# Kernel tuning notes

Measured on AMD Instinct MI355X. Metric: run time of the kernel, lower is better.

## Reference

```python
import jax, jax.numpy as jnp
import numpy as np

L, S, N, E, H = 2048, 2048, 4, 1024, 16
D = E // H


def setup_inputs() -> dict:
    k0 = jax.random.key(0)
    ks = jax.random.split(k0, 11)
    std = 1.0 / np.sqrt(E)
    return {
        "query": jax.random.normal(ks[0], (L, N, E), jnp.float32),
        "key": jax.random.normal(ks[1], (S, N, E), jnp.float32),
        "value": jax.random.normal(ks[2], (S, N, E), jnp.float32),
        "Wq": jax.random.normal(ks[3], (E, E), jnp.float32) * std,
        "bq": jnp.zeros((E,), jnp.float32),
        "Wk": jax.random.normal(ks[4], (E, E), jnp.float32) * std,
        "bk": jnp.zeros((E,), jnp.float32),
        "Wv": jax.random.normal(ks[5], (E, E), jnp.float32) * std,
        "bv": jnp.zeros((E,), jnp.float32),
        "Wo": jax.random.normal(ks[6], (E, E), jnp.float32) * std,
        "bo": jnp.zeros((E,), jnp.float32),
    }


def reference(query, key, value, Wq, bq, Wk, bk, Wv, bv, Wo, bo):
    # projections (torch Linear: x @ W.T + b)
    q = query @ Wq.T + bq  # [L,N,E]
    k = key @ Wk.T + bk    # [S,N,E]
    v = value @ Wv.T + bv  # [S,N,E]
    # split heads -> [N,H,len,D]
    q = q.reshape(L, N, H, D).transpose(1, 2, 0, 3)
    k = k.reshape(S, N, H, D).transpose(1, 2, 0, 3)
    v = v.reshape(S, N, H, D).transpose(1, 2, 0, 3)
    scores = jnp.einsum("nhld,nhsd->nhls", q, k) / np.sqrt(D).astype(np.float32)
    attn_weights = jax.nn.softmax(scores, axis=-1)  # [N,H,L,S]
    out = jnp.einsum("nhls,nhsd->nhld", attn_weights, v)  # [N,H,L,D]
    out = out.transpose(2, 0, 1, 3).reshape(L, N, E)
    attn_output = out @ Wo.T + bo  # [L,N,E]
    # need_weights=True, average_attn_weights=True -> mean over heads
    return attn_output, attn_weights.mean(axis=1)
```

## Files before the change

### kernel.cpp

```cpp
#include <hip/hip_runtime.h>
#include <hip/hip_bf16.h>

typedef __attribute__((ext_vector_type(8))) short short8;
typedef __attribute__((ext_vector_type(4))) float f32x4;

#define AS1 __attribute__((address_space(1)))
#define AS3 __attribute__((address_space(3)))

__device__ __forceinline__ void gload16(const void* g, void* l) {
  __builtin_amdgcn_global_load_lds((const AS1 unsigned int*)g,
                                   (AS3 unsigned int*)l, 16, 0, 0);
}

__device__ __forceinline__ unsigned short f2bf(float x) {
  unsigned u = __float_as_uint(x);
  u = (u + 0x7FFFu + ((u >> 16) & 1u)) >> 16;
  return (unsigned short)u;
}

__device__ __forceinline__ short8 lds8(const unsigned short* p) {
  return *(const short8*)p;
}

__device__ __forceinline__ short8 lds8s(const unsigned short* base, int row, int byteInRow) {
  const int a = (row << 7) + (byteInRow ^ ((row & 7) << 4));
  return *(const short8*)((const char*)base + a);
}

#define LL 2048
#define NB 4
#define EE 1024
#define HH 16
#define DD 64
#define MROWS 8192
#define SC2 0.18033688f
#define MFIX 16.0f

__global__ __launch_bounds__(256) void conv_bf16(const float* __restrict__ src,
                                                 unsigned short* __restrict__ dst) {
  int i = blockIdx.x * 256 + threadIdx.x;
  float4 v = ((const float4*)src)[i];
  ushort4 o;
  o.x = f2bf(v.x); o.y = f2bf(v.y); o.z = f2bf(v.z); o.w = f2bf(v.w);
  ((ushort4*)dst)[i] = o;
}

__global__ __launch_bounds__(256) void conv_w4(const float* __restrict__ s0,
                                               const float* __restrict__ s1,
                                               const float* __restrict__ s2,
                                               const float* __restrict__ s3,
                                               unsigned short* __restrict__ d0,
                                               unsigned short* __restrict__ d1,
                                               unsigned short* __restrict__ d2,
                                               unsigned short* __restrict__ d3) {
  const float* src;
  unsigned short* dst;
  switch (blockIdx.y) {
    case 0: src = s0; dst = d0; break;
    case 1: src = s1; dst = d1; break;
    case 2: src = s2; dst = d2; break;
    default: src = s3; dst = d3; break;
  }
  int i = blockIdx.x * 256 + threadIdx.x;
  float4 v = ((const float4*)src)[i];
  ushort4 o;
  o.x = f2bf(v.x); o.y = f2bf(v.y); o.z = f2bf(v.z); o.w = f2bf(v.w);
  ((ushort4*)dst)[i] = o;
}

template <int MODE>
__global__ __launch_bounds__(256) void gemm_bt(const unsigned short* __restrict__ A,
                                               const unsigned short* __restrict__ B,
                                               const float* __restrict__ bias,
                                               unsigned short* __restrict__ outb,
                                               float* __restrict__ outf) {
  constexpr int K = 1024;
  __shared__ __align__(16) unsigned short As[2][64 * 64];
  __shared__ __align__(16) unsigned short Bs[2][64 * 64];
  const int tid = threadIdx.x;
  const int lane = tid & 63, w = tid >> 6;
  const int wr = w >> 1, wc = w & 1;
  const int lrow = lane & 15, lg = lane >> 4;
  const int m0 = blockIdx.y * 128, n0 = blockIdx.x * 128;

  f32x4 acc[4][4] = {};

  const int sr = tid >> 3, sseg = tid & 7;
  const int slog = sseg ^ (sr & 7);
  const int mA = sr + 64 * (slog >> 2);
  const int kof = (slog & 3) * 8;
  const unsigned short* ga  = A + (size_t)(m0 + mA) * K + kof;
  const unsigned short* ga2 = A + (size_t)(m0 + mA + 32) * K + kof;
  const unsigned short* gb  = B + (size_t)(n0 + mA) * K + kof;
  const unsigned short* gb2 = B + (size_t)(n0 + mA + 32) * K + kof;

  gload16(ga,  (char*)As[0] + tid * 16);
  gload16(ga2, (char*)As[0] + tid * 16 + 4096);
  gload16(gb,  (char*)Bs[0] + tid * 16);
  gload16(gb2, (char*)Bs[0] + tid * 16 + 4096);
  __syncthreads();

  int cur = 0;
  for (int k0 = 0; k0 < K; k0 += 32) {
    if (k0 + 32 < K) {
      const int nxt = cur ^ 1;
      gload16(ga  + k0 + 32, (char*)As[nxt] + tid * 16);
      gload16(ga2 + k0 + 32, (char*)As[nxt] + tid * 16 + 4096);
      gload16(gb  + k0 + 32, (char*)Bs[nxt] + tid * 16);
      gload16(gb2 + k0 + 32, (char*)Bs[nxt] + tid * 16 + 4096);
    }

    short8 af[4], bfr[4];
#pragma unroll
    for (int mt = 0; mt < 4; ++mt)
      af[mt] = lds8s(As[cur], mt * 16 + lrow, (wr * 4 + lg) * 16);
#pragma unroll
    for (int nt = 0; nt < 4; ++nt)
      bfr[nt] = lds8s(Bs[cur], nt * 16 + lrow, (wc * 4 + lg) * 16);
#pragma unroll
    for (int mt = 0; mt < 4; ++mt)
#pragma unroll
      for (int nt = 0; nt < 4; ++nt)
        acc[mt][nt] = __builtin_amdgcn_mfma_f32_16x16x32_bf16(af[mt], bfr[nt],
                                                              acc[mt][nt], 0, 0, 0);
    __syncthreads();
    cur ^= 1;
  }

#pragma unroll
  for (int mt = 0; mt < 4; ++mt) {
#pragma unroll
    for (int nt = 0; nt < 4; ++nt) {
      const int col = n0 + wc * 64 + nt * 16 + lrow;
      const float bv = bias[col];
#pragma unroll
      for (int r = 0; r < 4; ++r) {
        const int row = m0 + wr * 64 + mt * 16 + lg * 4 + r;
        const float v = acc[mt][nt][r] + bv;
        if (MODE == 0) {
          const int l = row >> 2, n = row & 3, h = col >> 6, d = col & 63;
          outb[(((size_t)(n * HH + h)) * LL + l) * DD + d] = f2bf(v);
        } else if (MODE == 1) {
          const int s = row >> 2, n = row & 3, h = col >> 6, d = col & 63;
          outb[(((size_t)(n * HH + h)) * DD + d) * LL + s] = f2bf(v);
        } else {
          outf[(size_t)row * EE + col] = v;
        }
      }
    }
  }
}

__global__ __launch_bounds__(256) void flash_attn(const unsigned short* __restrict__ qh,
                                                  const unsigned short* __restrict__ kh,
                                                  const unsigned short* __restrict__ vth,
                                                  unsigned short* __restrict__ oh,
                                                  float* __restrict__ cT) {
  __shared__ __align__(16) unsigned short Ks[64 * 64];
  __shared__ __align__(16) unsigned short Vts[64 * 64];
  __shared__ __align__(16) unsigned short QPs[128 * 64];
  const int tid = threadIdx.x, lane = tid & 63, w = tid >> 6;
  const int lrow = lane & 15, lg = lane >> 4;
  const int flat = blockIdx.x + (blockIdx.y << 4);
  const int nh = ((flat >> 7) << 3) | (flat & 7);
  const int l0 = ((flat >> 3) & 15) * 128;

  const unsigned short* qbase = qh + ((size_t)nh * LL + l0) * DD;
  const unsigned short* kbase = kh + (size_t)nh * LL * DD;
  const unsigned short* vbase = vth + (size_t)nh * DD * LL;

  const int sr = tid >> 3;
  const int cs = ((tid & 7) ^ (sr & 7)) * 8;

#pragma unroll
  for (int c = 0; c < 4; ++c)
    gload16(qbase + (size_t)(c * 32 + sr) * DD + cs, (char*)QPs + c * 4096 + tid * 16);
  gload16(kbase + (size_t)sr * DD + cs,        (char*)Ks + tid * 16);
  gload16(kbase + (size_t)(sr + 32) * DD + cs, (char*)Ks + tid * 16 + 4096);
  gload16(vbase + (size_t)sr * LL + cs,        (char*)Vts + tid * 16);
  gload16(vbase + (size_t)(sr + 32) * LL + cs, (char*)Vts + tid * 16 + 4096);
  __syncthreads();

  short8 qa[2][2];
#pragma unroll
  for (int qs = 0; qs < 2; ++qs) {
    qa[qs][0] = lds8s(QPs, w * 32 + qs * 16 + lrow, lg * 16);
    qa[qs][1] = lds8s(QPs, w * 32 + qs * 16 + lrow, 64 + lg * 16);
  }

  const short onev = (short)0x3F80;
  const short8 ones = {onev, onev, onev, onev, onev, onev, onev, onev};
  const f32x4 fz = {};

  f32x4 acco[2][4] = {};
  f32x4 accz[2] = {};

  const unsigned short* kpre = kbase + (size_t)(64 + sr) * DD + cs;
  const unsigned short* vpre = vbase + (size_t)sr * LL + 64 + cs;

  const int prow0 = w * 32 + lrow;

#pragma unroll 1
  for (int t = 0; t < 32; ++t) {
    const bool pf = (t < 31);

    f32x4 sc0[4];
    __builtin_amdgcn_s_setprio(1);
#pragma unroll
    for (int ct = 0; ct < 4; ++ct) {
      short8 b0 = lds8s(Ks, ct * 16 + lrow, lg * 16);
      short8 b1 = lds8s(Ks, ct * 16 + lrow, 64 + lg * 16);
      sc0[ct] = __builtin_amdgcn_mfma_f32_16x16x32_bf16(
          b1, qa[0][1],
          __builtin_amdgcn_mfma_f32_16x16x32_bf16(b0, qa[0][0], fz, 0, 0, 0),
          0, 0, 0);
    }
    __builtin_amdgcn_s_setprio(0);

#pragma unroll
    for (int ct = 0; ct < 4; ++ct) {
      float e0 = __builtin_exp2f(__builtin_fmaf(sc0[ct][0], SC2, -MFIX));
      float e1 = __builtin_exp2f(__builtin_fmaf(sc0[ct][1], SC2, -MFIX));
      float e2 = __builtin_exp2f(__builtin_fmaf(sc0[ct][2], SC2, -MFIX));
      float e3 = __builtin_exp2f(__builtin_fmaf(sc0[ct][3], SC2, -MFIX));
      unsigned int p0, p1;
      asm("v_cvt_pk_bf16_f32 %0, %1, %2" : "=v"(p0) : "v"(e0), "v"(e1));
      asm("v_cvt_pk_bf16_f32 %0, %1, %2" : "=v"(p1) : "v"(e2), "v"(e3));
      const int a = (prow0 << 7) + ((((ct * 2 + (lg >> 1)) ^ (prow0 & 7)) << 4) | ((lg & 1) << 3));
      uint2 u; u.x = p0; u.y = p1;
      *(uint2*)((char*)QPs + a) = u;
    }

    f32x4 sc1[4];
    __builtin_amdgcn_s_setprio(1);
#pragma unroll
    for (int ct = 0; ct < 4; ++ct) {
      short8 b0 = lds8s(Ks, ct * 16 + lrow, lg * 16);
      short8 b1 = lds8s(Ks, ct * 16 + lrow, 64 + lg * 16);
      sc1[ct] = __builtin_amdgcn_mfma_f32_16x16x32_bf16(
          b1, qa[1][1],
          __builtin_amdgcn_mfma_f32_16x16x32_bf16(b0, qa[1][0], fz, 0, 0, 0),
          0, 0, 0);
    }
    __builtin_amdgcn_s_setprio(0);

    __syncthreads();
    if (pf) {
      gload16(kpre,                   (char*)Ks + tid * 16);
      gload16(kpre + (size_t)32 * DD, (char*)Ks + tid * 16 + 4096);
      kpre += (size_t)64 * DD;
    }

    const int prow1 = prow0 + 16;
#pragma unroll
    for (int ct = 0; ct < 4; ++ct) {
      float e0 = __builtin_exp2f(__builtin_fmaf(sc1[ct][0], SC2, -MFIX));
      float e1 = __builtin_exp2f(__builtin_fmaf(sc1[ct][1], SC2, -MFIX));
      float e2 = __builtin_exp2f(__builtin_fmaf(sc1[ct][2], SC2, -MFIX));
      float e3 = __builtin_exp2f(__builtin_fmaf(sc1[ct][3], SC2, -MFIX));
      unsigned int p0, p1;
      asm("v_cvt_pk_bf16_f32 %0, %1, %2" : "=v"(p0) : "v"(e0), "v"(e1));
      asm("v_cvt_pk_bf16_f32 %0, %1, %2" : "=v"(p1) : "v"(e2), "v"(e3));
      const int a = (prow1 << 7) + ((((ct * 2 + (lg >> 1)) ^ (prow1 & 7)) << 4) | ((lg & 1) << 3));
      uint2 u; u.x = p0; u.y = p1;
      *(uint2*)((char*)QPs + a) = u;
    }

    short8 pa00 = lds8s(QPs, prow0, lg * 16);
    short8 pa01 = lds8s(QPs, prow0, 64 + lg * 16);
    short8 pa10 = lds8s(QPs, prow1, lg * 16);
    short8 pa11 = lds8s(QPs, prow1, 64 + lg * 16);
    __builtin_amdgcn_s_setprio(1);
#pragma unroll
    for (int dt = 0; dt < 4; ++dt) {
      short8 vb0 = lds8s(Vts, dt * 16 + lrow, lg * 16);
      short8 vb1 = lds8s(Vts, dt * 16 + lrow, 64 + lg * 16);
      acco[0][dt] = __builtin_amdgcn_mfma_f32_16x16x32_bf16(vb0, pa00, acco[0][dt], 0, 0, 0);
      acco[0][dt] = __builtin_amdgcn_mfma_f32_16x16x32_bf16(vb1, pa01, acco[0][dt], 0, 0, 0);
      acco[1][dt] = __builtin_amdgcn_mfma_f32_16x16x32_bf16(vb0, pa10, acco[1][dt], 0, 0, 0);
      acco[1][dt] = __builtin_amdgcn_mfma_f32_16x16x32_bf16(vb1, pa11, acco[1][dt], 0, 0, 0);
    }
    accz[0] = __builtin_amdgcn_mfma_f32_16x16x32_bf16(ones, pa00, accz[0], 0, 0, 0);
    accz[0] = __builtin_amdgcn_mfma_f32_16x16x32_bf16(ones, pa01, accz[0], 0, 0, 0);
    accz[1] = __builtin_amdgcn_mfma_f32_16x16x32_bf16(ones, pa10, accz[1], 0, 0, 0);
    accz[1] = __builtin_amdgcn_mfma_f32_16x16x32_bf16(ones, pa11, accz[1], 0, 0, 0);
    __builtin_amdgcn_s_setprio(0);

    __syncthreads();
    if (pf) {
      gload16(vpre,                   (char*)Vts + tid * 16);
      gload16(vpre + (size_t)32 * LL, (char*)Vts + tid * 16 + 4096);
      vpre += 64;
    }
  }

  const int n = nh >> 4, h = nh & 15;
#pragma unroll
  for (int qs = 0; qs < 2; ++qs) {
    const int lt = l0 + w * 32 + qs * 16 + lrow;
    const float zrow = accz[qs][0];
    const float rz = 1.0f / zrow;
#pragma unroll
    for (int dt = 0; dt < 4; ++dt) {
      ushort4 o;
      o.x = f2bf(acco[qs][dt][0] * rz);
      o.y = f2bf(acco[qs][dt][1] * rz);
      o.z = f2bf(acco[qs][dt][2] * rz);
      o.w = f2bf(acco[qs][dt][3] * rz);
      *(ushort4*)&oh[((size_t)lt * NB + n) * EE + h * 64 + dt * 16 + lg * 4] = o;
    }
    if (lg == 0) {
      cT[((size_t)n * LL + lt) * HH + h] = -(MFIX + __builtin_log2f(zrow));
    }
  }
}

__global__ __launch_bounds__(256) void weights_mean(const unsigned short* __restrict__ qh,
                                                    const unsigned short* __restrict__ kh,
                                                    const float* __restrict__ cT,
                                                    float* __restrict__ out1) {
  __shared__ __align__(16) unsigned short Qs[64 * 64];
  __shared__ __align__(16) unsigned short Ks[64 * 64];
  const int tid = threadIdx.x, lane = tid & 63, w = tid >> 6;
  const int lrow = lane & 15, lg = lane >> 4;
  const int n = blockIdx.z;
  const int l0 = blockIdx.y * 64, s0 = blockIdx.x * 64;

  const int sr = tid >> 3;
  const int cs = ((tid & 7) ^ (sr & 7)) * 8;
  const f32x4 fz = {};

  float accw[4][4] = {};
  for (int h = 0; h < HH; ++h) {
    const int nh = n * HH + h;
    __syncthreads();
    const unsigned short* qbase = qh + ((size_t)nh * LL + l0) * DD;
    const unsigned short* kbase = kh + ((size_t)nh * LL + s0) * DD;
    gload16(qbase + (size_t)sr * DD + cs,        (char*)Qs + tid * 16);
    gload16(qbase + (size_t)(sr + 32) * DD + cs, (char*)Qs + tid * 16 + 4096);
    gload16(kbase + (size_t)sr * DD + cs,        (char*)Ks + tid * 16);
    gload16(kbase + (size_t)(sr + 32) * DD + cs, (char*)Ks + tid * 16 + 4096);
    __syncthreads();

    short8 qa0 = lds8s(Qs, w * 16 + lrow, lg * 16);
    short8 qa1 = lds8s(Qs, w * 16 + lrow, 64 + lg * 16);
    f32x4 sc[4];
    __builtin_amdgcn_s_setprio(1);
#pragma unroll
    for (int ct = 0; ct < 4; ++ct) {
      short8 b0 = lds8s(Ks, ct * 16 + lrow, lg * 16);
      short8 b1 = lds8s(Ks, ct * 16 + lrow, 64 + lg * 16);
      sc[ct] = __builtin_amdgcn_mfma_f32_16x16x32_bf16(
          qa1, b1,
          __builtin_amdgcn_mfma_f32_16x16x32_bf16(qa0, b0, fz, 0, 0, 0),
          0, 0, 0);
    }
    __builtin_amdgcn_s_setprio(0);
#pragma unroll
    for (int r = 0; r < 4; ++r) {
      const int lt = l0 + w * 16 + lg * 4 + r;
      const float c = cT[((size_t)n * LL + lt) * HH + h];
#pragma unroll
      for (int ct = 0; ct < 4; ++ct)
        accw[ct][r] += __builtin_exp2f(__builtin_fmaf(sc[ct][r], SC2, c));
    }
  }
#pragma unroll
  for (int ct = 0; ct < 4; ++ct)
#pragma unroll
    for (int r = 0; r < 4; ++r) {
      const int lt = l0 + w * 16 + lg * 4 + r;
      const int s = s0 + ct * 16 + lrow;
      out1[((size_t)n * LL + lt) * LL + s] = accw[ct][r] * 0.0625f;
    }
}

extern "C" void kernel_launch(void* const* d_in, const int* in_sizes, int n_in,
                              void* d_out, int out_size, void* d_ws, size_t ws_size,
                              hipStream_t stream) {
  const float* query = (const float*)d_in[0];
  const float* key   = (const float*)d_in[1];
  const float* value = (const float*)d_in[2];
  const float* Wq = (const float*)d_in[3];
  const float* bq = (const float*)d_in[4];
  const float* Wk = (const float*)d_in[5];
  const float* bk = (const float*)d_in[6];
  const float* Wv = (const float*)d_in[7];
  const float* bv = (const float*)d_in[8];
  const float* Wo = (const float*)d_in[9];
  const float* bo = (const float*)d_in[10];

  float* out0 = (float*)d_out;
  float* out1 = out0 + (size_t)LL * NB * EE;

  char* ws = (char*)d_ws;
  unsigned short* xbuf = (unsigned short*)(ws + 0);
  unsigned short* wqb  = (unsigned short*)(ws + 16777216);
  unsigned short* wkb  = (unsigned short*)(ws + 18874368);
  unsigned short* wvb  = (unsigned short*)(ws + 20971520);
  unsigned short* wob  = (unsigned short*)(ws + 23068672);
  unsigned short* qhb  = (unsigned short*)(ws + 25165824);
  unsigned short* khb  = (unsigned short*)(ws + 41943040);
  unsigned short* vthb = (unsigned short*)(ws + 58720256);
  float* cT   = (float*)(ws + 75497472);

  const int nTok = MROWS * EE;
  const int nW   = EE * EE;

  conv_w4<<<dim3(nW / 1024, 4), 256, 0, stream>>>(Wq, Wk, Wv, Wo, wqb, wkb, wvb, wob);

  dim3 ggrid(EE / 128, MROWS / 128);

  conv_bf16<<<nTok / 1024, 256, 0, stream>>>(query, xbuf);
  gemm_bt<0><<<ggrid, 256, 0, stream>>>(xbuf, wqb, bq, qhb, nullptr);
  conv_bf16<<<nTok / 1024, 256, 0, stream>>>(key, xbuf);
  gemm_bt<0><<<ggrid, 256, 0, stream>>>(xbuf, wkb, bk, khb, nullptr);
  conv_bf16<<<nTok / 1024, 256, 0, stream>>>(value, xbuf);
  gemm_bt<1><<<ggrid, 256, 0, stream>>>(xbuf, wvb, bv, vthb, nullptr);

  flash_attn<<<dim3(LL / 128, NB * HH), 256, 0, stream>>>(qhb, khb, vthb, xbuf, cT);

  gemm_bt<2><<<ggrid, 256, 0, stream>>>(xbuf, wob, bo, nullptr, out0);

  weights_mean<<<dim3(LL / 64, LL / 64, NB), 256, 0, stream>>>(qhb, khb, cT, out1);
}
```

Before: 371.7 us.

## Split attention over key dimension into two halves with combine kernel

Launches flash attention with a second grid dimension that splits the key/value sequence into two halves, doubling block count, and each half writes unnormalized bf16 partial outputs and partial row sums. A new combine kernel sums the two partials, normalizes, and writes the log-normalizer used by the weights kernel. This aims to improve GPU occupancy and load balance, at the cost of an extra kernel, extra memory traffic, and bf16 rounding of unnormalized partials. Scratch buffers are placed inside unused regions of the output tensors.

New measurement: 378.0 us. Within noise of the previous version (+1.7%).

```diff
diff --git a/kernel.cpp b/kernel.cpp
--- a/kernel.cpp
+++ b/kernel.cpp
@@ -16,6 +16,10 @@
   unsigned u = __float_as_uint(x);
   u = (u + 0x7FFFu + ((u >> 16) & 1u)) >> 16;
   return (unsigned short)u;
+}
+
+__device__ __forceinline__ float bf2f(unsigned short u) {
+  return __uint_as_float((unsigned)u << 16);
 }
 
 __device__ __forceinline__ short8 lds8(const unsigned short* p) {
@@ -154,8 +158,10 @@
 __global__ __launch_bounds__(256) void flash_attn(const unsigned short* __restrict__ qh,
                                                   const unsigned short* __restrict__ kh,
                                                   const unsigned short* __restrict__ vth,
-                                                  unsigned short* __restrict__ oh,
-                                                  float* __restrict__ cT) {
+                                                  unsigned short* __restrict__ po0,
+                                                  unsigned short* __restrict__ po1,
+                                                  float* __restrict__ zp0,
+                                                  float* __restrict__ zp1) {
   __shared__ __align__(16) unsigned short Ks[64 * 64];
   __shared__ __align__(16) unsigned short Vts[64 * 64];
   __shared__ __align__(16) unsigned short QPs[128 * 64];
@@ -164,10 +170,14 @@
   const int flat = blockIdx.x + (blockIdx.y << 4);
   const int nh = ((flat >> 7) << 3) | (flat & 7);
   const int l0 = ((flat >> 3) & 15) * 128;
+  const int sh = blockIdx.z;
+  unsigned short* po = sh ? po1 : po0;
+  float* zp = sh ? zp1 : zp0;
+  const int sbase = sh * (LL / 2);
 
   const unsigned short* qbase = qh + ((size_t)nh * LL + l0) * DD;
-  const unsigned short* kbase = kh + (size_t)nh * LL * DD;
-  const unsigned short* vbase = vth + (size_t)nh * DD * LL;
+  const unsigned short* kbase = kh + ((size_t)nh * LL + sbase) * DD;
+  const unsigned short* vbase = vth + (size_t)nh * DD * LL + sbase;
 
   const int sr = tid >> 3;
   const int cs = ((tid & 7) ^ (sr & 7)) * 8;
@@ -201,8 +211,8 @@
   const int prow0 = w * 32 + lrow;
 
 #pragma unroll 1
-  for (int t = 0; t < 32; ++t) {
-    const bool pf = (t < 31);
+  for (int t = 0; t < 16; ++t) {
+    const bool pf = (t < 15);
 
     f32x4 sc0[4];
     __builtin_amdgcn_s_setprio(1);
@@ -298,21 +308,44 @@
 #pragma unroll
   for (int qs = 0; qs < 2; ++qs) {
     const int lt = l0 + w * 32 + qs * 16 + lrow;
-    const float zrow = accz[qs][0];
-    const float rz = 1.0f / zrow;
 #pragma unroll
     for (int dt = 0; dt < 4; ++dt) {
       ushort4 o;
-      o.x = f2bf(acco[qs][dt][0] * rz);
-      o.y = f2bf(acco[qs][dt][1] * rz);
-      o.z = f2bf(acco[qs][dt][2] * rz);
-      o.w = f2bf(acco[qs][dt][3] * rz);
-      *(ushort4*)&oh[((size_t)lt * NB + n) * EE + h * 64 + dt * 16 + lg * 4] = o;
-    }
-    if (lg == 0) {
-      cT[((size_t)n * LL + lt) * HH + h] = -(MFIX + __builtin_log2f(zrow));
-    }
-  }
+      o.x = f2bf(acco[qs][dt][0]);
+      o.y = f2bf(acco[qs][dt][1]);
+      o.z = f2bf(acco[qs][dt][2]);
+      o.w = f2bf(acco[qs][dt][3]);
+      *(ushort4*)&po[((size_t)lt * NB + n) * EE + h * 64 + dt * 16 + lg * 4] = o;
+    }
+    if (lg == 0) zp[(size_t)nh * LL + lt] = accz[qs][0];
+  }
+}
+
+__global__ __launch_bounds__(256) void combine_o(const unsigned short* __restrict__ po1,
+                                                 const float* __restrict__ z0,
+                                                 const float* __restrict__ z1,
+                                                 unsigned short* __restrict__ oh,
+                                                 float* __restrict__ cT) {
+  const int j = blockIdx.x * 256 + threadIdx.x;
+  const int f = j * 4;
+  const int col = f & 1023;
+  const int n = (f >> 10) & 3;
+  const int lt = f >> 12;
+  const int h = col >> 6;
+  const int nh = n * HH + h;
+  const float za = z0[(size_t)nh * LL + lt], zb = z1[(size_t)nh * LL + lt];
+  const float zs = za + zb;
+  const float rz = 1.0f / zs;
+  ushort4 a = ((const ushort4*)oh)[j];
+  ushort4 b = ((const ushort4*)po1)[j];
+  ushort4 o;
+  o.x = f2bf((bf2f(a.x) + bf2f(b.x)) * rz);
+  o.y = f2bf((bf2f(a.y) + bf2f(b.y)) * rz);
+  o.z = f2bf((bf2f(a.z) + bf2f(b.z)) * rz);
+  o.w = f2bf((bf2f(a.w) + bf2f(b.w)) * rz);
+  ((ushort4*)oh)[j] = o;
+  if ((col & 63) == 0)
+    cT[((size_t)n * LL + lt) * HH + h] = -(MFIX + __builtin_log2f(zs));
 }
 
 __global__ __launch_bounds__(256) void weights_mean(const unsigned short* __restrict__ qh,
@@ -404,6 +437,10 @@
   unsigned short* vthb = (unsigned short*)(ws + 58720256);
   float* cT   = (float*)(ws + 75497472);
 
+  unsigned short* po1 = (unsigned short*)((char*)out1 + 33554432);
+  float* z0 = (float*)((char*)out0 + 16777216);
+  float* z1 = (float*)((char*)out0 + 18874368);
+
   const int nTok = MROWS * EE;
   const int nW   = EE * EE;
 
@@ -418,7 +455,9 @@
   conv_bf16<<<nTok / 1024, 256, 0, stream>>>(value, xbuf);
   gemm_bt<1><<<ggrid, 256, 0, stream>>>(xbuf, wvb, bv, vthb, nullptr);
 
-  flash_attn<<<dim3(LL / 128, NB * HH), 256, 0, stream>>>(qhb, khb, vthb, xbuf, cT);
+  flash_attn<<<dim3(LL / 128, NB * HH, 2), 256, 0, stream>>>(qhb, khb, vthb,
+                                                             xbuf, po1, z0, z1);
+  combine_o<<<nTok / 4 / 256, 256, 0, stream>>>(po1, z0, z1, xbuf, cT);
 
   gemm_bt<2><<<ggrid, 256, 0, stream>>>(xbuf, wob, bo, nullptr, out0);
 
```
